# Performance work log

Hardware: AMD Instinct MI355X
Metric: run time of the kernel (lower is better)

## Reference

```python
import jax, jax.numpy as jnp
import numpy as np

B, T, I, H = 256, 512, 64, 256


def _lstm_layer(x, Wih, Whh, bih, bhh):
    # x: [B, T, in], Wih: [4H, in], Whh: [4H, H], biases: [4H]
    # PyTorch gate order: i, f, g, o.  c' = f*c + i*g ; h = o*tanh(c')
    Hd = Whh.shape[1]
    xp = jnp.einsum('bti,gi->btg', x, Wih) + bih + bhh  # [B, T, 4H]
    h0 = jnp.zeros((x.shape[0], Hd), x.dtype)
    c0 = jnp.zeros((x.shape[0], Hd), x.dtype)

    def step(carry, xt):
        h, c = carry
        g = xt + h @ Whh.T
        i, f, gg, o = jnp.split(g, 4, axis=-1)
        i = jax.nn.sigmoid(i)
        f = jax.nn.sigmoid(f)
        gg = jnp.tanh(gg)
        o = jax.nn.sigmoid(o)
        c = f * c + i * gg
        h = o * jnp.tanh(c)
        return (h, c), h

    _, hs = jax.lax.scan(step, (h0, c0), jnp.swapaxes(xp, 0, 1))  # [T, B, H]
    return jnp.swapaxes(hs, 0, 1)


def setup_inputs() -> dict:
    key = jax.random.key(0)
    ks = jax.random.split(key, 20)
    s_in = 1.0 / np.sqrt(I)
    s_h = 1.0 / np.sqrt(H)
    d = {
        'x': jax.random.normal(ks[0], (B, T, I), jnp.float32),
        # encoder layer 0: input I -> H
        'enc_Wih0': jax.random.normal(ks[1], (4 * H, I), jnp.float32) * s_in,
        'enc_Whh0': jax.random.normal(ks[2], (4 * H, H), jnp.float32) * s_h,
        'enc_bih0': jnp.zeros((4 * H,), jnp.float32),
        'enc_bhh0': jnp.zeros((4 * H,), jnp.float32),
        # encoder layer 1: H -> H
        'enc_Wih1': jax.random.normal(ks[3], (4 * H, H), jnp.float32) * s_h,
        'enc_Whh1': jax.random.normal(ks[4], (4 * H, H), jnp.float32) * s_h,
        'enc_bih1': jnp.zeros((4 * H,), jnp.float32),
        'enc_bhh1': jnp.zeros((4 * H,), jnp.float32),
        # decoder layer 0: H -> H
        'dec_Wih0': jax.random.normal(ks[5], (4 * H, H), jnp.float32) * s_h,
        'dec_Whh0': jax.random.normal(ks[6], (4 * H, H), jnp.float32) * s_h,
        'dec_bih0': jnp.zeros((4 * H,), jnp.float32),
        'dec_bhh0': jnp.zeros((4 * H,), jnp.float32),
        # decoder layer 1: H -> H
        'dec_Wih1': jax.random.normal(ks[7], (4 * H, H), jnp.float32) * s_h,
        'dec_Whh1': jax.random.normal(ks[8], (4 * H, H), jnp.float32) * s_h,
        'dec_bih1': jnp.zeros((4 * H,), jnp.float32),
        'dec_bhh1': jnp.zeros((4 * H,), jnp.float32),
        # output projection H -> I
        'out_W': jax.random.normal(ks[9], (I, H), jnp.float32) * s_h,
        'out_b': jnp.zeros((I,), jnp.float32),
    }
    return d


def reference(x,
              enc_Wih0, enc_Whh0, enc_bih0, enc_bhh0,
              enc_Wih1, enc_Whh1, enc_bih1, enc_bhh1,
              dec_Wih0, dec_Whh0, dec_bih0, dec_bhh0,
              dec_Wih1, dec_Whh1, dec_bih1, dec_bhh1,
              out_W, out_b):
    # Encoder (2 stacked LSTM layers, inference mode -> no inter-layer dropout)
    h = _lstm_layer(x, enc_Wih0, enc_Whh0, enc_bih0, enc_bhh0)
    encoded = _lstm_layer(h, enc_Wih1, enc_Whh1, enc_bih1, enc_bhh1)
    # Decoder (2 stacked LSTM layers over the encoded sequence)
    h = _lstm_layer(encoded, dec_Wih0, dec_Whh0, dec_bih0, dec_bhh0)
    decoded_hidden = _lstm_layer(h, dec_Wih1, dec_Whh1, dec_bih1, dec_bhh1)
    # Linear projection back to input_size
    reconstruction = jnp.einsum('bth,ih->bti', decoded_hidden, out_W) + out_b
    return reconstruction
```

## Files before the change

kernel.cpp:

```cpp
#include <hip/hip_runtime.h>

typedef unsigned short u16;
typedef unsigned int   u32;
typedef _Float16 f16;
typedef _Float16 half2v __attribute__((ext_vector_type(2)));
typedef _Float16 half8v __attribute__((ext_vector_type(8)));
typedef float float4v __attribute__((ext_vector_type(4)));

#define B_  256
#define T_  512
#define I_  64
#define H_  256
#define G_  1024
#define BT_ (B_*T_)

static __device__ __forceinline__ float fdot2u(u32 a, u32 b, float c) {
#if defined(__has_builtin) && __has_builtin(__builtin_amdgcn_fdot2)
  return __builtin_amdgcn_fdot2(__builtin_bit_cast(half2v, a),
                                __builtin_bit_cast(half2v, b), c, false);
#else
  half2v av = __builtin_bit_cast(half2v, a), bv = __builtin_bit_cast(half2v, b);
  return c + (float)av.x * (float)bv.x + (float)av.y * (float)bv.y;
#endif
}

static __device__ __forceinline__ float sig_(float x) {
  return 1.0f / (1.0f + __expf(-x));
}
static __device__ __forceinline__ float tanh_(float x) {
  float ax = fminf(fabsf(x), 15.0f);
  float e  = __expf(2.0f * ax);
  float t  = (e - 1.0f) / (e + 1.0f);
  return copysignf(t, x);
}


__global__ void cvt_f16(const float* __restrict__ in, u16* __restrict__ out, int n) {
  int i = blockIdx.x * blockDim.x + threadIdx.x;
  if (i < n) out[i] = __builtin_bit_cast(u16, (f16)in[i]);
}

__global__ void split_w(const float* __restrict__ w, u16* __restrict__ hi,
                        u16* __restrict__ lo, int n) {
  int i = blockIdx.x * blockDim.x + threadIdx.x;
  if (i < n) {
    float v = w[i];
    f16 h = (f16)v;
    float r = v - (float)h;
    hi[i] = __builtin_bit_cast(u16, h);
    lo[i] = __builtin_bit_cast(u16, (f16)r);
  }
}

__global__ void bias_sum(const float* __restrict__ a, const float* __restrict__ b,
                         float* __restrict__ o, int n) {
  int i = blockIdx.x * blockDim.x + threadIdx.x;
  if (i < n) o[i] = a[i] + b[i];
}

template<int BN>
__global__ __launch_bounds__(256) void gemm_ws(
    const u16* __restrict__ A, const u16* __restrict__ Bh, const u16* __restrict__ Bl,
    const float* __restrict__ bias, float* __restrict__ C,
    int K, int tcl, int t0, int N)
{
  constexpr int BM = 128, BK = 64, LDT = 72;
  __shared__ u16 As[BM * LDT];
  __shared__ u16 Bhs[BN * LDT];
  __shared__ u16 Bls[BN * LDT];
  const int tid = threadIdx.x, wave = tid >> 6, lane = tid & 63;
  const int m0 = blockIdx.x * BM, n0 = blockIdx.y * BN;
  constexpr int WNT = BN / 32;
  const int wm0 = (wave >> 1) * 64, wn0 = (wave & 1) * (BN / 2);
  const int tcmask = (1 << tcl) - 1;
  float4v acc[4][WNT];
  for (int i = 0; i < 4; i++)
    for (int j = 0; j < WNT; j++) acc[i][j] = (float4v){0.f, 0.f, 0.f, 0.f};
  const int lrow = lane & 15, lk = (lane >> 4) * 8;

  for (int k0 = 0; k0 < K; k0 += BK) {
    __syncthreads();
#pragma unroll
    for (int i = 0; i < 4; i++) {
      int idx = tid + i * 256, row = idx >> 3, u = idx & 7;
      int m = m0 + row;
      int rg = (m >> tcl) * T_ + t0 + (m & tcmask);
      *(uint4*)(As + row * LDT + u * 8) =
          *(const uint4*)(A + (size_t)rg * K + k0 + u * 8);
    }
#pragma unroll
    for (int i = 0; i < WNT; i++) {
      int idx = tid + i * 256, row = idx >> 3, u = idx & 7;
      size_t go = (size_t)(n0 + row) * K + k0 + u * 8;
      *(uint4*)(Bhs + row * LDT + u * 8) = *(const uint4*)(Bh + go);
      *(uint4*)(Bls + row * LDT + u * 8) = *(const uint4*)(Bl + go);
    }
    __syncthreads();
#pragma unroll
    for (int ks = 0; ks < 2; ++ks) {
      int col = ks * 32 + lk;
      half8v af[4];
#pragma unroll
      for (int mt = 0; mt < 4; mt++)
        af[mt] = *(const half8v*)(const void*)(As + (wm0 + mt * 16 + lrow) * LDT + col);
#pragma unroll
      for (int nt = 0; nt < WNT; nt++) {
        half8v bhv = *(const half8v*)(const void*)(Bhs + (wn0 + nt * 16 + lrow) * LDT + col);
        half8v blv = *(const half8v*)(const void*)(Bls + (wn0 + nt * 16 + lrow) * LDT + col);
#pragma unroll
        for (int mt = 0; mt < 4; mt++) {
          acc[mt][nt] = __builtin_amdgcn_mfma_f32_16x16x32_f16(af[mt], bhv, acc[mt][nt], 0, 0, 0);
          acc[mt][nt] = __builtin_amdgcn_mfma_f32_16x16x32_f16(af[mt], blv, acc[mt][nt], 0, 0, 0);
        }
      }
    }
  }
  const int crow = (lane >> 4) * 4, ccol = lane & 15;
#pragma unroll
  for (int nt = 0; nt < WNT; nt++) {
    int n = n0 + wn0 + nt * 16 + ccol;
    float bv = bias[n];
#pragma unroll
    for (int mt = 0; mt < 4; mt++) {
#pragma unroll
      for (int r = 0; r < 4; r++) {
        int m = m0 + wm0 + mt * 16 + crow + r;
        C[(size_t)m * N + n] = acc[mt][nt][r] + bv;
      }
    }
  }
}

__global__ __launch_bounds__(512, 2) void lstm_scan(
    const u16* __restrict__ whh, const float* __restrict__ xp,
    u16* __restrict__ hout, float* __restrict__ cst, u16* __restrict__ hst,
    int Tc, int t0)
{
  __shared__ u16 wt[1024 * 72];
  __shared__ float gs[1024];
  __shared__ u32 h2s[128];
  const int tid = threadIdx.x, b = blockIdx.x;
  const int r0 = tid, r1 = tid + 512;

  uint4 w0q[24], w1q[24];
  const uint4* g0 = (const uint4*)(whh + (size_t)r0 * 256);
  const uint4* g1 = (const uint4*)(whh + (size_t)r1 * 256);
#pragma unroll
  for (int i = 0; i < 24; i++) { w0q[i] = g0[i]; w1q[i] = g1[i]; }
#pragma unroll
  for (int i = 0; i < 8; i++) {
    *((uint4*)(wt + (size_t)r0 * 72) + i) = g0[24 + i];
    *((uint4*)(wt + (size_t)r1 * 72) + i) = g1[24 + i];
  }

  float cc = 0.f;
  if (t0 == 0) {
    if (tid < 128) h2s[tid] = 0u;
  } else {
    if (tid < 256) cc = cst[(size_t)b * 256 + tid];
    if (tid < 128) h2s[tid] = ((const u32*)hst)[(size_t)b * 128 + tid];
  }
  __syncthreads();

  const float* xpb = xp + (size_t)b * Tc * 1024;
  float xn0 = xpb[r0], xn1 = xpb[r1];
  u16* houtb = hout + (size_t)b * T_ * 256 + (size_t)t0 * 256;

  for (int tt = 0; tt < Tc; ++tt) {
    float a0 = xn0, a1 = xn1;
    if (tt + 1 < Tc) {
      xn0 = xpb[(size_t)(tt + 1) * 1024 + r0];
      xn1 = xpb[(size_t)(tt + 1) * 1024 + r1];
    }
    const uint4* hq = (const uint4*)h2s;
#pragma unroll
    for (int kc = 0; kc < 24; ++kc) {
      uint4 hv = hq[kc];
      uint4 w0 = w0q[kc], w1 = w1q[kc];
      a0 = fdot2u(w0.x, hv.x, a0); a0 = fdot2u(w0.y, hv.y, a0);
      a0 = fdot2u(w0.z, hv.z, a0); a0 = fdot2u(w0.w, hv.w, a0);
      a1 = fdot2u(w1.x, hv.x, a1); a1 = fdot2u(w1.y, hv.y, a1);
      a1 = fdot2u(w1.z, hv.z, a1); a1 = fdot2u(w1.w, hv.w, a1);
    }
    const uint4* wt0 = (const uint4*)(wt + (size_t)r0 * 72);
    const uint4* wt1 = (const uint4*)(wt + (size_t)r1 * 72);
#pragma unroll
    for (int kc = 0; kc < 8; ++kc) {
      uint4 hv = hq[24 + kc];
      uint4 w0 = wt0[kc], w1 = wt1[kc];
      a0 = fdot2u(w0.x, hv.x, a0); a0 = fdot2u(w0.y, hv.y, a0);
      a0 = fdot2u(w0.z, hv.z, a0); a0 = fdot2u(w0.w, hv.w, a0);
      a1 = fdot2u(w1.x, hv.x, a1); a1 = fdot2u(w1.y, hv.y, a1);
      a1 = fdot2u(w1.z, hv.z, a1); a1 = fdot2u(w1.w, hv.w, a1);
    }
    gs[r0] = a0; gs[r1] = a1;
    __syncthreads();
    if (tid < 256) {
      float gi = gs[tid], gf = gs[tid + 256], gg = gs[tid + 512], go = gs[tid + 768];
      float iv = sig_(gi), fv = sig_(gf), ov = sig_(go), gv = tanh_(gg);
      cc = fv * cc + iv * gv;
      float hv = ov * tanh_(cc);
      u16 hb = __builtin_bit_cast(u16, (f16)hv);
      ((u16*)h2s)[tid] = hb;
      houtb[(size_t)tt * 256 + tid] = hb;
    }
    __syncthreads();
  }
  if (tid < 256) cst[(size_t)b * 256 + tid] = cc;
  if (tid < 128) ((u32*)hst)[(size_t)b * 128 + tid] = h2s[tid];
}


extern "C" void kernel_launch(void* const* d_in, const int* in_sizes, int n_in,
                              void* d_out, int out_size, void* d_ws, size_t ws_size,
                              hipStream_t stream)
{
  const float* x      = (const float*)d_in[0];
  const float* Wih[4] = {(const float*)d_in[1], (const float*)d_in[5],
                         (const float*)d_in[9], (const float*)d_in[13]};
  const float* Whh[4] = {(const float*)d_in[2], (const float*)d_in[6],
                         (const float*)d_in[10], (const float*)d_in[14]};
  const float* bi[4]  = {(const float*)d_in[3], (const float*)d_in[7],
                         (const float*)d_in[11], (const float*)d_in[15]};
  const float* bh[4]  = {(const float*)d_in[4], (const float*)d_in[8],
                         (const float*)d_in[12], (const float*)d_in[16]};
  const float* outW   = (const float*)d_in[17];
  const float* outb   = (const float*)d_in[18];

  char* ws = (char*)d_ws;
  size_t off = 0;
  auto alc = [&](size_t bytes) -> char* {
    char* p = ws + off;
    off = (off + bytes + 255) & ~(size_t)255;
    return p;
  };

  u16* xf  = (u16*)alc((size_t)BT_ * I_ * 2);
  u16* hb0 = (u16*)alc((size_t)BT_ * H_ * 2);
  u16* hb1 = (u16*)alc((size_t)BT_ * H_ * 2);
  int wihn[4] = {G_ * I_, G_ * H_, G_ * H_, G_ * H_};
  u16 *wihH[4], *wihL[4], *whhH[4];
  float* bsum[4];
  for (int l = 0; l < 4; l++) {
    wihH[l] = (u16*)alc((size_t)wihn[l] * 2);
    wihL[l] = (u16*)alc((size_t)wihn[l] * 2);
    whhH[l] = (u16*)alc((size_t)G_ * H_ * 2);
    bsum[l] = (float*)alc((size_t)G_ * 4);
  }
  u16* owH = (u16*)alc((size_t)I_ * H_ * 2);
  u16* owL = (u16*)alc((size_t)I_ * H_ * 2);
  float* cst = (float*)alc((size_t)B_ * H_ * 4);
  u16*   hst = (u16*)alc((size_t)B_ * H_ * 2);

  int Tc = T_;
  while (Tc > 16 && off + (size_t)B_ * Tc * G_ * 4 + 4096 > ws_size) Tc >>= 1;
  float* xpb = (float*)alc((size_t)B_ * Tc * G_ * 4);
  int tcl = 0;
  while ((1 << tcl) < Tc) tcl++;

  {
    int n = BT_ * I_;
    cvt_f16<<<dim3((n + 255) / 256), dim3(256), 0, stream>>>(x, xf, n);
  }
  for (int l = 0; l < 4; l++) {
    split_w<<<dim3((wihn[l] + 255) / 256), dim3(256), 0, stream>>>(Wih[l], wihH[l], wihL[l], wihn[l]);
    cvt_f16<<<dim3((G_ * H_ + 255) / 256), dim3(256), 0, stream>>>(Whh[l], whhH[l], G_ * H_);
    bias_sum<<<dim3(4), dim3(256), 0, stream>>>(bi[l], bh[l], bsum[l], G_);
  }
  split_w<<<dim3((I_ * H_ + 255) / 256), dim3(256), 0, stream>>>(outW, owH, owL, I_ * H_);

  for (int l = 0; l < 4; l++) {
    const u16* Ain = (l == 0) ? xf : ((l == 1) ? hb0 : (l == 2) ? hb1 : hb0);
    u16* Hout = (l & 1) ? hb1 : hb0;
    int K = (l == 0) ? I_ : H_;
    for (int t0 = 0; t0 < T_; t0 += Tc) {
      gemm_ws<128><<<dim3((B_ * Tc) / 128, G_ / 128), dim3(256), 0, stream>>>(
          Ain, wihH[l], wihL[l], bsum[l], xpb, K, tcl, t0, G_);
      lstm_scan<<<dim3(B_), dim3(512), 0, stream>>>(whhH[l], xpb, Hout, cst, hst, Tc, t0);
    }
  }

  gemm_ws<64><<<dim3(BT_ / 128, 1), dim3(256), 0, stream>>>(
      hb1, owH, owL, outb, (float*)d_out, H_, 9, 0, I_);
}
```

Before: 4.979 ms.

## Compute all four gates per thread and double-buffer hidden state in LSTM scan

The recurrent scan kernel now uses 256 threads per block, and each thread computes all four gate pre-activations for one hidden unit, so the gate exchange through shared memory and one of the two per-step barriers go away. The hidden state is double-buffered in shared memory so a single barrier per timestep is enough. The cost is heavier register pressure (96 uint4 of weights per thread), half as many threads per block, and a different shared-memory weight layout, which could cause register spills or lower occupancy.

```diff
diff --git a/kernel.cpp b/kernel.cpp
--- a/kernel.cpp
+++ b/kernel.cpp
@@ -131,83 +131,88 @@
   }
 }
 
-__global__ __launch_bounds__(512, 2) void lstm_scan(
+__global__ __launch_bounds__(256, 1) void lstm_scan(
     const u16* __restrict__ whh, const float* __restrict__ xp,
     u16* __restrict__ hout, float* __restrict__ cst, u16* __restrict__ hst,
     int Tc, int t0)
 {
-  __shared__ u16 wt[1024 * 72];
-  __shared__ float gs[1024];
-  __shared__ u32 h2s[128];
+  __shared__ u16 wt[32 * 256 * 8];
+  __shared__ u32 hbuf[2][128];
   const int tid = threadIdx.x, b = blockIdx.x;
-  const int r0 = tid, r1 = tid + 512;
-
-  uint4 w0q[24], w1q[24];
-  const uint4* g0 = (const uint4*)(whh + (size_t)r0 * 256);
-  const uint4* g1 = (const uint4*)(whh + (size_t)r1 * 256);
-#pragma unroll
-  for (int i = 0; i < 24; i++) { w0q[i] = g0[i]; w1q[i] = g1[i]; }
-#pragma unroll
-  for (int i = 0; i < 8; i++) {
-    *((uint4*)(wt + (size_t)r0 * 72) + i) = g0[24 + i];
-    *((uint4*)(wt + (size_t)r1 * 72) + i) = g1[24 + i];
+
+  uint4 w[4][24];
+#pragma unroll
+  for (int g = 0; g < 4; g++) {
+    const uint4* gp = (const uint4*)(whh + (size_t)(g * 256 + tid) * 256);
+#pragma unroll
+    for (int i = 0; i < 24; i++) w[g][i] = gp[i];
+#pragma unroll
+    for (int q = 0; q < 8; q++)
+      *(uint4*)(wt + ((size_t)(g * 8 + q) * 256 + tid) * 8) = gp[24 + q];
   }
 
   float cc = 0.f;
   if (t0 == 0) {
-    if (tid < 128) h2s[tid] = 0u;
+    if (tid < 128) hbuf[0][tid] = 0u;
   } else {
-    if (tid < 256) cc = cst[(size_t)b * 256 + tid];
-    if (tid < 128) h2s[tid] = ((const u32*)hst)[(size_t)b * 128 + tid];
+    cc = cst[(size_t)b * 256 + tid];
+    if (tid < 128) hbuf[0][tid] = ((const u32*)hst)[(size_t)b * 128 + tid];
   }
   __syncthreads();
 
   const float* xpb = xp + (size_t)b * Tc * 1024;
-  float xn0 = xpb[r0], xn1 = xpb[r1];
-  u16* houtb = hout + (size_t)b * T_ * 256 + (size_t)t0 * 256;
-
+  float xn[4];
+#pragma unroll
+  for (int g = 0; g < 4; g++) xn[g] = xpb[g * 256 + tid];
+  u16* houtb = hout + ((size_t)b * T_ + t0) * 256;
+
+  u16 hb = 0;
   for (int tt = 0; tt < Tc; ++tt) {
-    float a0 = xn0, a1 = xn1;
+    float a0 = xn[0], a1 = xn[1], a2 = xn[2], a3 = xn[3];
     if (tt + 1 < Tc) {
-      xn0 = xpb[(size_t)(tt + 1) * 1024 + r0];
-      xn1 = xpb[(size_t)(tt + 1) * 1024 + r1];
-    }
-    const uint4* hq = (const uint4*)h2s;
+#pragma unroll
+      for (int g = 0; g < 4; g++)
+        xn[g] = xpb[(size_t)(tt + 1) * 1024 + g * 256 + tid];
+    }
+    const uint4* hq = (const uint4*)hbuf[tt & 1];
 #pragma unroll
     for (int kc = 0; kc < 24; ++kc) {
       uint4 hv = hq[kc];
-      uint4 w0 = w0q[kc], w1 = w1q[kc];
+      a0 = fdot2u(w[0][kc].x, hv.x, a0); a0 = fdot2u(w[0][kc].y, hv.y, a0);
+      a0 = fdot2u(w[0][kc].z, hv.z, a0); a0 = fdot2u(w[0][kc].w, hv.w, a0);
+      a1 = fdot2u(w[1][kc].x, hv.x, a1); a1 = fdot2u(w[1][kc].y, hv.y, a1);
+      a1 = fdot2u(w[1][kc].z, hv.z, a1); a1 = fdot2u(w[1][kc].w, hv.w, a1);
+      a2 = fdot2u(w[2][kc].x, hv.x, a2); a2 = fdot2u(w[2][kc].y, hv.y, a2);
+      a2 = fdot2u(w[2][kc].z, hv.z, a2); a2 = fdot2u(w[2][kc].w, hv.w, a2);
+      a3 = fdot2u(w[3][kc].x, hv.x, a3); a3 = fdot2u(w[3][kc].y, hv.y, a3);
+      a3 = fdot2u(w[3][kc].z, hv.z, a3); a3 = fdot2u(w[3][kc].w, hv.w, a3);
+    }
+#pragma unroll
+    for (int q = 0; q < 8; ++q) {
+      uint4 hv = hq[24 + q];
+      uint4 w0 = *(const uint4*)(wt + ((size_t)(0 * 8 + q) * 256 + tid) * 8);
+      uint4 w1 = *(const uint4*)(wt + ((size_t)(1 * 8 + q) * 256 + tid) * 8);
+      uint4 w2 = *(const uint4*)(wt + ((size_t)(2 * 8 + q) * 256 + tid) * 8);
+      uint4 w3 = *(const uint4*)(wt + ((size_t)(3 * 8 + q) * 256 + tid) * 8);
       a0 = fdot2u(w0.x, hv.x, a0); a0 = fdot2u(w0.y, hv.y, a0);
       a0 = fdot2u(w0.z, hv.z, a0); a0 = fdot2u(w0.w, hv.w, a0);
       a1 = fdot2u(w1.x, hv.x, a1); a1 = fdot2u(w1.y, hv.y, a1);
       a1 = fdot2u(w1.z, hv.z, a1); a1 = fdot2u(w1.w, hv.w, a1);
-    }
-    const uint4* wt0 = (const uint4*)(wt + (size_t)r0 * 72);
-    const uint4* wt1 = (const uint4*)(wt + (size_t)r1 * 72);
-#pragma unroll
-    for (int kc = 0; kc < 8; ++kc) {
-      uint4 hv = hq[24 + kc];
-      uint4 w0 = wt0[kc], w1 = wt1[kc];
-      a0 = fdot2u(w0.x, hv.x, a0); a0 = fdot2u(w0.y, hv.y, a0);
-      a0 = fdot2u(w0.z, hv.z, a0); a0 = fdot2u(w0.w, hv.w, a0);
-      a1 = fdot2u(w1.x, hv.x, a1); a1 = fdot2u(w1.y, hv.y, a1);
-      a1 = fdot2u(w1.z, hv.z, a1); a1 = fdot2u(w1.w, hv.w, a1);
-    }
-    gs[r0] = a0; gs[r1] = a1;
+      a2 = fdot2u(w2.x, hv.x, a2); a2 = fdot2u(w2.y, hv.y, a2);
+      a2 = fdot2u(w2.z, hv.z, a2); a2 = fdot2u(w2.w, hv.w, a2);
+      a3 = fdot2u(w3.x, hv.x, a3); a3 = fdot2u(w3.y, hv.y, a3);
+      a3 = fdot2u(w3.z, hv.z, a3); a3 = fdot2u(w3.w, hv.w, a3);
+    }
+    float iv = sig_(a0), fv = sig_(a1), gv = tanh_(a2), ov = sig_(a3);
+    cc = fv * cc + iv * gv;
+    float hval = ov * tanh_(cc);
+    hb = __builtin_bit_cast(u16, (f16)hval);
+    ((u16*)hbuf[(tt + 1) & 1])[tid] = hb;
+    houtb[(size_t)tt * 256 + tid] = hb;
     __syncthreads();
-    if (tid < 256) {
-      float gi = gs[tid], gf = gs[tid + 256], gg = gs[tid + 512], go = gs[tid + 768];
-      float iv = sig_(gi), fv = sig_(gf), ov = sig_(go), gv = tanh_(gg);
-      cc = fv * cc + iv * gv;
-      float hv = ov * tanh_(cc);
-      u16 hb = __builtin_bit_cast(u16, (f16)hv);
-      ((u16*)h2s)[tid] = hb;
-      houtb[(size_t)tt * 256 + tid] = hb;
-    }
-    __syncthreads();
-  }
-  if (tid < 256) cst[(size_t)b * 256 + tid] = cc;
-  if (tid < 128) ((u32*)hst)[(size_t)b * 128 + tid] = h2s[tid];
+  }
+  cst[(size_t)b * 256 + tid] = cc;
+  hst[(size_t)b * 256 + tid] = hb;
 }
 
 
@@ -276,7 +281,7 @@
     for (int t0 = 0; t0 < T_; t0 += Tc) {
       gemm_ws<128><<<dim3((B_ * Tc) / 128, G_ / 128), dim3(256), 0, stream>>>(
           Ain, wihH[l], wihL[l], bsum[l], xpb, K, tcl, t0, G_);
-      lstm_scan<<<dim3(B_), dim3(512), 0, stream>>>(whhH[l], xpb, Hout, cst, hst, Tc, t0);
+      lstm_scan<<<dim3(B_), dim3(256), 0, stream>>>(whhH[l], xpb, Hout, cst, hst, Tc, t0);
     }
   }
 
```

New measurement: 8.142 ms. 63.5% more time.
